# Optimization experiments

Measured on AMD Instinct MI355X. Metric: run time of the kernel, lower is better.

Reference implementation:

```python
import jax, jax.numpy as jnp
import numpy as np

# DeepSpeed FixedSparsityConfig defaults (attention='unidirectional')
BLOCK = 16
NUM_LOCAL_BLOCKS = 4   # local window = 4 blocks = 64 tokens
D_MODEL = 1024
N_HEADS = 16
HEAD_DIM = D_MODEL // N_HEADS


def _block_layout(seq_len: int) -> np.ndarray:
    """Token-level boolean mask [S,S] from the fixed unidirectional block layout.
    Allowed iff: (same 4-block local window AND block_k <= block_q) OR
                 (block_k % 4 == 3 AND block_k <= block_q)  (causal global column).
    Same layout for every head (different_layout_per_head=False)."""
    nb = seq_len // BLOCK
    r = np.arange(nb)
    causal = r[None, :] <= r[:, None]
    same_win = (r[:, None] // NUM_LOCAL_BLOCKS) == (r[None, :] // NUM_LOCAL_BLOCKS)
    glob = (r[None, :] % NUM_LOCAL_BLOCKS) == (NUM_LOCAL_BLOCKS - 1)
    layout = (same_win & causal) | (glob & causal)
    return np.kron(layout, np.ones((BLOCK, BLOCK), dtype=bool))


def setup_inputs() -> dict:
    key = jax.random.key(0)
    ks = jax.random.split(key, 7)
    B, S = 2, 2048
    init = 1.0 / np.sqrt(D_MODEL)
    x = jax.random.normal(ks[0], (B, S, D_MODEL), jnp.float32)
    key_padding_mask = jnp.zeros((B, S), jnp.float32)  # additive mask ('add' mode)
    Wq = jax.random.normal(ks[1], (D_MODEL, D_MODEL), jnp.float32) * init
    Wk = jax.random.normal(ks[2], (D_MODEL, D_MODEL), jnp.float32) * init
    Wv = jax.random.normal(ks[3], (D_MODEL, D_MODEL), jnp.float32) * init
    bq = jax.random.normal(ks[4], (D_MODEL,), jnp.float32) * 0.01
    bk = jax.random.normal(ks[5], (D_MODEL,), jnp.float32) * 0.01
    bv = jax.random.normal(ks[6], (D_MODEL,), jnp.float32) * 0.01
    return dict(x=x, key_padding_mask=key_padding_mask,
                Wq=Wq, bq=bq, Wk=Wk, bk=bk, Wv=Wv, bv=bv)


def reference(x, key_padding_mask, Wq, bq, Wk, bk, Wv, bv):
    B, S, D = x.shape
    q = (x @ Wq + bq).reshape(B, S, N_HEADS, HEAD_DIM)
    k = (x @ Wk + bk).reshape(B, S, N_HEADS, HEAD_DIM)
    v = (x @ Wv + bv).reshape(B, S, N_HEADS, HEAD_DIM)
    scale = HEAD_DIM ** -0.5  # DeepSpeed scales by head_size**-0.5 inside softmax
    scores = jnp.einsum('bqhd,bkhd->bhqk', q, k) * scale
    scores = scores + key_padding_mask[:, None, None, :]
    mask = jnp.asarray(_block_layout(S))  # [S,S] bool; absent blocks excluded from softmax
    scores = jnp.where(mask[None, None], scores, -jnp.inf)
    attn = jax.nn.softmax(scores, axis=-1)
    out = jnp.einsum('bhqk,bkhd->bqhd', attn, v)
    return out.reshape(B, S, D)
```

## Files before the change

kernel.cpp:

```cpp
#include <hip/hip_runtime.h>
#include <hip/hip_bf16.h>

typedef __bf16 bf16;
typedef __bf16 bf16x4 __attribute__((ext_vector_type(4)));
typedef __bf16 bf16x8 __attribute__((ext_vector_type(8)));
typedef float  f32x4  __attribute__((ext_vector_type(4)));

#define D_MODEL 1024
#define S_LEN   2048
#define BATCH   2
#define NH      16
#define HD      64
#define NX ((size_t)BATCH * S_LEN * D_MODEL)

__device__ inline void gl_lds16(const bf16* g, bf16* l) {
    __builtin_amdgcn_global_load_lds(
        (const __attribute__((address_space(1))) void*)g,
        (__attribute__((address_space(3))) void*)l, 16, 0, 0);
}

__global__ __launch_bounds__(256) void prep(
    const float* __restrict__ x, bf16* __restrict__ xb,
    const float* __restrict__ Wq, const float* __restrict__ Wk,
    const float* __restrict__ Wv, bf16* __restrict__ Wt)
{
    __shared__ bf16 tile[64 * 72];

    if (blockIdx.x < 2048) {
        const size_t base = ((size_t)blockIdx.x * 256 + threadIdx.x) * 8;
        const float4 a = *(const float4*)(x + base);
        const float4 b = *(const float4*)(x + base + 4);
        bf16x8 o;
        o[0] = (bf16)a.x; o[1] = (bf16)a.y; o[2] = (bf16)a.z; o[3] = (bf16)a.w;
        o[4] = (bf16)b.x; o[5] = (bf16)b.y; o[6] = (bf16)b.z; o[7] = (bf16)b.w;
        *(bf16x8*)(xb + base) = o;
        return;
    }

    const int id2 = blockIdx.x - 2048;
    const int z = id2 >> 8;
    const float* W = (z == 0) ? Wq : (z == 1) ? Wk : Wv;
    const int k0 = ((id2 >> 4) & 15) * 64, n0 = (id2 & 15) * 64;

    const int r16 = threadIdx.x >> 4, c4 = (threadIdx.x & 15) << 2;

#pragma unroll
    for (int rr = 0; rr < 4; ++rr) {
        const int row = rr * 16 + r16;
        const float4 v = *(const float4*)(W + (size_t)(k0 + row) * D_MODEL + n0 + c4);
        bf16x4 o; o[0] = (bf16)v.x; o[1] = (bf16)v.y; o[2] = (bf16)v.z; o[3] = (bf16)v.w;
        *(bf16x4*)(tile + row * 72 + c4) = o;
    }
    __syncthreads();
#pragma unroll
    for (int rr = 0; rr < 4; ++rr) {
        const int row = rr * 16 + r16;
        bf16x4 o;
#pragma unroll
        for (int j = 0; j < 4; ++j) o[j] = tile[(c4 + j) * 72 + row];
        *(bf16x4*)(Wt + (size_t)(z * D_MODEL + n0 + row) * D_MODEL + k0 + c4) = o;
    }
}

#define GNT 32

__device__ __forceinline__ void stage_128(
    const bf16* __restrict__ src, bf16* __restrict__ dst,
    int row0, int k0, int tid, int wave)
{
    const int ci0 = tid;
    const int r0 = ci0 >> 2, c0 = (ci0 & 3) ^ ((ci0 >> 3) & 3);
    gl_lds16(src + (size_t)(row0 + r0) * D_MODEL + k0 + c0 * 8, dst + wave * 512);
    const int ci1 = 256 + tid;
    const int r1 = ci1 >> 2, c1 = (ci1 & 3) ^ ((ci1 >> 3) & 3);
    gl_lds16(src + (size_t)(row0 + r1) * D_MODEL + k0 + c1 * 8, dst + 2048 + wave * 512);
}

template<int VM>
__device__ __forceinline__ void gemm_tile_body(
    const bf16* __restrict__ Xb, const bf16* __restrict__ Wt,
    bf16* __restrict__ As, bf16* __restrict__ Bs,
    int m0, int n0, int t, int tid, int wave, int wm, int wn,
    int col, int pchunk, f32x4 (&acc)[4][4])
{
    __builtin_amdgcn_sched_barrier(0);
    if constexpr (VM == 4) asm volatile("s_waitcnt vmcnt(4)");
    else                   asm volatile("s_waitcnt vmcnt(0)");
    __builtin_amdgcn_sched_barrier(0);
    __builtin_amdgcn_s_barrier();
    __builtin_amdgcn_sched_barrier(0);

    const int cur = t % 3;
    const bf16* bufA = As + cur * 4096;
    const bf16* bufB = Bs + cur * 4096;

    if (t + 2 < GNT) {
        const int nslot = (t + 2) % 3;
        const int k2 = (t + 2) * 32;
        stage_128(Xb, As + nslot * 4096, m0, k2, tid, wave);
        stage_128(Wt, Bs + nslot * 4096, n0, k2, tid, wave);
    }

    bf16x8 a[4], b[4];
#pragma unroll
    for (int mr = 0; mr < 4; ++mr)
        a[mr] = *(const bf16x8*)(bufA + (wm * 64 + mr * 16 + col) * 32 + pchunk * 8);
#pragma unroll
    for (int nr = 0; nr < 4; ++nr)
        b[nr] = *(const bf16x8*)(bufB + (wn * 64 + nr * 16 + col) * 32 + pchunk * 8);

#pragma unroll
    for (int mr = 0; mr < 4; ++mr)
#pragma unroll
        for (int nr = 0; nr < 4; ++nr)
            acc[mr][nr] = __builtin_amdgcn_mfma_f32_16x16x32_bf16(a[mr], b[nr], acc[mr][nr], 0, 0, 0);
}

__global__ __launch_bounds__(256, 3) void gemm_qkv_dp(
    const bf16* __restrict__ Xb, const bf16* __restrict__ Wt,
    const float* __restrict__ bq, const float* __restrict__ bk,
    const float* __restrict__ bv, bf16* __restrict__ QKV)
{
    extern __shared__ bf16 smem[];
    bf16* As = smem;
    bf16* Bs = smem + 12288;

    const int bid = blockIdx.x, k = bid & 7, j = bid >> 3;
    const int my = ((k & 3) << 3) + (j & 7);
    const int nx = ((k >> 2) * 12) + (j >> 3);
    const int m0 = my * 128, n0 = nx * 128;

    const int tid = threadIdx.x, wave = tid >> 6, lane = tid & 63;
    const int wm = wave >> 1, wn = wave & 1;
    const int col = lane & 15, quad = lane >> 4;
    const int pchunk = quad ^ ((col >> 1) & 3);

    f32x4 acc[4][4] = {};

    stage_128(Xb, As,        m0,  0, tid, wave);
    stage_128(Wt, Bs,        n0,  0, tid, wave);
    stage_128(Xb, As + 4096, m0, 32, tid, wave);
    stage_128(Wt, Bs + 4096, n0, 32, tid, wave);

    for (int t = 0; t < GNT - 1; ++t)
        gemm_tile_body<4>(Xb, Wt, As, Bs, m0, n0, t, tid, wave, wm, wn, col, pchunk, acc);
    gemm_tile_body<0>(Xb, Wt, As, Bs, m0, n0, GNT - 1, tid, wave, wm, wn, col, pchunk, acc);

    const int z = n0 >> 10, nc0 = n0 & 1023;
    const float* bias = (z == 0) ? bq : (z == 1) ? bk : bv;
    const float scale = (z == 0) ? 0.125f : 1.0f;
    bf16* C = QKV + (size_t)z * NX;
#pragma unroll
    for (int nr = 0; nr < 4; ++nr) {
        const int c = nc0 + wn * 64 + nr * 16 + col;
        const float bsv = bias[c];
#pragma unroll
        for (int mr = 0; mr < 4; ++mr)
#pragma unroll
            for (int i = 0; i < 4; ++i) {
                const int rg = m0 + wm * 64 + mr * 16 + quad * 4 + i;
                C[(size_t)rg * D_MODEL + c] = (bf16)((acc[mr][nr][i] + bsv) * scale);
            }
    }
}

__global__ __launch_bounds__(256, 4) void sparse_attn64(
    const bf16* __restrict__ Q, const bf16* __restrict__ Kv,
    const bf16* __restrict__ Vv, const float* __restrict__ kpm,
    float* __restrict__ out)
{
    const int lid = blockIdx.x + 32 * (blockIdx.y + 16 * blockIdx.z);
    const int xk = lid & 7, j = lid >> 3;
    const int pair = xk * 4 + (j & 3);
    const int h = pair & 15, b = pair >> 4;
    const int w = 31 - (j >> 2);

    const int t = threadIdx.x, wavei = t >> 6, lane = t & 63;
    const int col = lane & 15, quad = lane >> 4;
    const int qb = 4 * w + wavei;

    __shared__ bf16 KbS[64 * 72];
    __shared__ bf16 VtS[2][64 * 72];
    __shared__ bf16 Ps[4][16 * 72];

    const size_t qrow = ((size_t)(b * S_LEN + qb * 16 + col)) * D_MODEL + h * HD;
    const bf16x8 aq0 = *(const bf16x8*)(Q + qrow + quad * 8);
    const bf16x8 aq1 = *(const bf16x8*)(Q + qrow + 32 + quad * 8);

    f32x4 o[4] = {};
    float lacc[4] = {0.f, 0.f, 0.f, 0.f};

    const int nGlob = (w + 3) >> 2;
    const int niter = nGlob + 1;

    const int srow = t >> 2, sd16 = (t & 3) << 4;
    const int sg = srow >> 4, sr = srow & 15;
    const int p2 = t & 31, dg8 = (t >> 5) << 3;
    const int key0 = 2 * p2, vg = key0 >> 4, vr = key0 & 15;

    auto kb_of = [&](int it, int g) -> int {
        if (it >= nGlob) return 4 * w + g;
        const int jj = 4 * it + g;
        return (jj < w) ? (4 * jj + 3) : 3;
    };

    bf16x8 rk0, rk1, rv0, rv1;
    {
        const size_t krow = ((size_t)(b * S_LEN + kb_of(0, sg) * 16 + sr)) * D_MODEL + h * HD + sd16;
        rk0 = *(const bf16x8*)(Kv + krow);
        rk1 = *(const bf16x8*)(Kv + krow + 8);
        const size_t vrow = ((size_t)(b * S_LEN + kb_of(0, vg) * 16 + vr)) * D_MODEL + h * HD + dg8;
        rv0 = *(const bf16x8*)(Vv + vrow);
        rv1 = *(const bf16x8*)(Vv + vrow + D_MODEL);
        *(bf16x8*)(KbS + srow * 72 + sd16)     = rk0;
        *(bf16x8*)(KbS + srow * 72 + sd16 + 8) = rk1;
#pragma unroll
        for (int jj = 0; jj < 8; ++jj) {
            bf16 pr[2] = { rv0[jj], rv1[jj] };
            *(unsigned int*)(VtS[0] + (dg8 + jj) * 72 + key0) = *(unsigned int*)pr;
        }
    }

    for (int it = 0; it < niter; ++it) {
        __syncthreads();
        const int cur = it & 1, nxt = cur ^ 1;
        const bool more = (it + 1 < niter);
        if (more) {
            const size_t krow = ((size_t)(b * S_LEN + kb_of(it + 1, sg) * 16 + sr)) * D_MODEL + h * HD + sd16;
            rk0 = *(const bf16x8*)(Kv + krow);
            rk1 = *(const bf16x8*)(Kv + krow + 8);
            const size_t vrow = ((size_t)(b * S_LEN + kb_of(it + 1, vg) * 16 + vr)) * D_MODEL + h * HD + dg8;
            rv0 = *(const bf16x8*)(Vv + vrow);
            rv1 = *(const bf16x8*)(Vv + vrow + D_MODEL);
        }

        f32x4 s[4];
        float mval[4];
        bool  val[4];
#pragma unroll
        for (int g = 0; g < 4; ++g) {
            val[g] = (it == nGlob) ? (g <= wavei) : (4 * it + g < w);
            if (val[g]) {
                const int kb = kb_of(it, g);
                mval[g] = kpm[b * S_LEN + kb * 16 + col];
                f32x4 z = {};
                const bf16x8 bk0 = *(const bf16x8*)(KbS + (g * 16 + col) * 72 + quad * 8);
                const bf16x8 bk1 = *(const bf16x8*)(KbS + (g * 16 + col) * 72 + 32 + quad * 8);
                __builtin_amdgcn_s_setprio(1);
                z = __builtin_amdgcn_mfma_f32_16x16x32_bf16(aq0, bk0, z, 0, 0, 0);
                s[g] = __builtin_amdgcn_mfma_f32_16x16x32_bf16(aq1, bk1, z, 0, 0, 0);
                __builtin_amdgcn_s_setprio(0);
            }
        }

        __syncthreads();
        if (more) {
            *(bf16x8*)(KbS + srow * 72 + sd16)     = rk0;
            *(bf16x8*)(KbS + srow * 72 + sd16 + 8) = rk1;
        }

#pragma unroll
        for (int g = 0; g < 4; ++g) {
            if (val[g]) {
#pragma unroll
                for (int i = 0; i < 4; ++i) {
                    const float pv = __expf(s[g][i] + mval[g]);
                    lacc[i] += pv;
                    Ps[wavei][(quad * 4 + i) * 72 + g * 16 + col] = (bf16)pv;
                }
            } else {
#pragma unroll
                for (int i = 0; i < 4; ++i)
                    Ps[wavei][(quad * 4 + i) * 72 + g * 16 + col] = (bf16)0.0f;
            }
        }

        const bf16* Vt = VtS[cur];
        const bf16x8 aP0 = *(const bf16x8*)(Ps[wavei] + col * 72 + quad * 8);
        const bf16x8 aP1 = *(const bf16x8*)(Ps[wavei] + col * 72 + 32 + quad * 8);
        __builtin_amdgcn_s_setprio(1);
#pragma unroll
        for (int nt = 0; nt < 4; ++nt) {
            const bf16x8 b0 = *(const bf16x8*)(Vt + (nt * 16 + col) * 72 + quad * 8);
            const bf16x8 b1 = *(const bf16x8*)(Vt + (nt * 16 + col) * 72 + 32 + quad * 8);
            o[nt] = __builtin_amdgcn_mfma_f32_16x16x32_bf16(aP0, b0, o[nt], 0, 0, 0);
            o[nt] = __builtin_amdgcn_mfma_f32_16x16x32_bf16(aP1, b1, o[nt], 0, 0, 0);
        }
        __builtin_amdgcn_s_setprio(0);

        if (more) {
#pragma unroll
            for (int jj = 0; jj < 8; ++jj) {
                bf16 pr[2] = { rv0[jj], rv1[jj] };
                *(unsigned int*)(VtS[nxt] + (dg8 + jj) * 72 + key0) = *(unsigned int*)pr;
            }
        }
    }

#pragma unroll
    for (int i = 0; i < 4; ++i) {
        float rs = lacc[i];
        rs += __shfl_xor(rs, 1);
        rs += __shfl_xor(rs, 2);
        rs += __shfl_xor(rs, 4);
        rs += __shfl_xor(rs, 8);
        const float inv = 1.0f / rs;
        const int rg = b * S_LEN + qb * 16 + quad * 4 + i;
#pragma unroll
        for (int nt = 0; nt < 4; ++nt)
            out[(size_t)rg * D_MODEL + h * HD + nt * 16 + col] = o[nt][i] * inv;
    }
}

extern "C" void kernel_launch(void* const* d_in, const int* in_sizes, int n_in,
                              void* d_out, int out_size, void* d_ws, size_t ws_size,
                              hipStream_t stream)
{
    const float* x = nullptr; const float* kpm = nullptr;
    const float* Wp[3] = {nullptr, nullptr, nullptr};
    const float* bp[3] = {nullptr, nullptr, nullptr};
    int wn = 0, bn = 0;
    for (int i = 0; i < n_in; ++i) {
        const float* p = (const float*)d_in[i];
        const long s = in_sizes[i];
        if (s == (long)NX)            x = p;
        else if (s == BATCH * S_LEN)  kpm = p;
        else if (s == D_MODEL * D_MODEL && wn < 3) Wp[wn++] = p;
        else if (s == D_MODEL && bn < 3)           bp[bn++] = p;
    }

    bf16* Qb = (bf16*)d_ws;
    bf16* Kb = Qb + NX;
    bf16* Vb = Kb + NX;
    bf16* Xb = (bf16*)d_out;
    bf16* Wt = Xb + NX;
    float* outp = (float*)d_out;

    static bool attr_done = false;
    if (!attr_done) {
        (void)hipFuncSetAttribute(reinterpret_cast<const void*>(gemm_qkv_dp),
                                  hipFuncAttributeMaxDynamicSharedMemorySize, 49152);
        attr_done = true;
    }

    prep<<<2816, 256, 0, stream>>>(x, Xb, Wp[0], Wp[1], Wp[2], Wt);

    gemm_qkv_dp<<<dim3(768), 256, 49152, stream>>>(
        Xb, Wt, bp[0], bp[1], bp[2], Qb);

    sparse_attn64<<<dim3(S_LEN / 64, NH, BATCH), 256, 0, stream>>>(
        Qb, Kb, Vb, kpm, outp);
}
```

Before: 141.8 us.

## Enlarge QKV GEMM tile to 256x192 so the grid fits one wave of CUs

```diff
diff --git a/kernel.cpp b/kernel.cpp
--- a/kernel.cpp
+++ b/kernel.cpp
@@ -64,16 +64,30 @@
 
 #define GNT 32
 
-__device__ __forceinline__ void stage_128(
+__device__ __forceinline__ void stage_A256(
     const bf16* __restrict__ src, bf16* __restrict__ dst,
     int row0, int k0, int tid, int wave)
 {
-    const int ci0 = tid;
-    const int r0 = ci0 >> 2, c0 = (ci0 & 3) ^ ((ci0 >> 3) & 3);
-    gl_lds16(src + (size_t)(row0 + r0) * D_MODEL + k0 + c0 * 8, dst + wave * 512);
-    const int ci1 = 256 + tid;
-    const int r1 = ci1 >> 2, c1 = (ci1 & 3) ^ ((ci1 >> 3) & 3);
-    gl_lds16(src + (size_t)(row0 + r1) * D_MODEL + k0 + c1 * 8, dst + 2048 + wave * 512);
+#pragma unroll
+    for (int p = 0; p < 4; ++p) {
+        const int ci = p * 256 + tid;
+        const int r = ci >> 2, c = (ci & 3) ^ ((ci >> 3) & 3);
+        gl_lds16(src + (size_t)(row0 + r) * D_MODEL + k0 + c * 8,
+                 dst + p * 2048 + wave * 512);
+    }
+}
+
+__device__ __forceinline__ void stage_B192(
+    const bf16* __restrict__ src, bf16* __restrict__ dst,
+    int row0, int k0, int tid, int wave)
+{
+#pragma unroll
+    for (int p = 0; p < 3; ++p) {
+        const int ci = p * 256 + tid;
+        const int r = ci >> 2, c = (ci & 3) ^ ((ci >> 3) & 3);
+        gl_lds16(src + (size_t)(row0 + r) * D_MODEL + k0 + c * 8,
+                 dst + p * 2048 + wave * 512);
+    }
 }
 
 template<int VM>
@@ -81,84 +95,82 @@
     const bf16* __restrict__ Xb, const bf16* __restrict__ Wt,
     bf16* __restrict__ As, bf16* __restrict__ Bs,
     int m0, int n0, int t, int tid, int wave, int wm, int wn,
-    int col, int pchunk, f32x4 (&acc)[4][4])
+    int col, int pchunk, f32x4 (&acc)[8][6])
 {
     __builtin_amdgcn_sched_barrier(0);
-    if constexpr (VM == 4) asm volatile("s_waitcnt vmcnt(4)");
+    if constexpr (VM == 7) asm volatile("s_waitcnt vmcnt(7)");
     else                   asm volatile("s_waitcnt vmcnt(0)");
     __builtin_amdgcn_sched_barrier(0);
     __builtin_amdgcn_s_barrier();
     __builtin_amdgcn_sched_barrier(0);
 
-    const int cur = t % 3;
-    const bf16* bufA = As + cur * 4096;
-    const bf16* bufB = Bs + cur * 4096;
+    const bf16* bufA = As + (t % 3) * 8192;
+    const bf16* bufB = Bs + (t % 3) * 6144;
 
     if (t + 2 < GNT) {
         const int nslot = (t + 2) % 3;
         const int k2 = (t + 2) * 32;
-        stage_128(Xb, As + nslot * 4096, m0, k2, tid, wave);
-        stage_128(Wt, Bs + nslot * 4096, n0, k2, tid, wave);
-    }
-
-    bf16x8 a[4], b[4];
-#pragma unroll
-    for (int mr = 0; mr < 4; ++mr)
-        a[mr] = *(const bf16x8*)(bufA + (wm * 64 + mr * 16 + col) * 32 + pchunk * 8);
-#pragma unroll
-    for (int nr = 0; nr < 4; ++nr)
-        b[nr] = *(const bf16x8*)(bufB + (wn * 64 + nr * 16 + col) * 32 + pchunk * 8);
-
-#pragma unroll
-    for (int mr = 0; mr < 4; ++mr)
-#pragma unroll
-        for (int nr = 0; nr < 4; ++nr)
+        stage_A256(Xb, As + nslot * 8192, m0, k2, tid, wave);
+        stage_B192(Wt, Bs + nslot * 6144, n0, k2, tid, wave);
+    }
+
+    bf16x8 a[8], b[6];
+#pragma unroll
+    for (int mr = 0; mr < 8; ++mr)
+        a[mr] = *(const bf16x8*)(bufA + (wm * 128 + mr * 16 + col) * 32 + pchunk * 8);
+#pragma unroll
+    for (int nr = 0; nr < 6; ++nr)
+        b[nr] = *(const bf16x8*)(bufB + (wn * 96 + nr * 16 + col) * 32 + pchunk * 8);
+
+#pragma unroll
+    for (int mr = 0; mr < 8; ++mr)
+#pragma unroll
+        for (int nr = 0; nr < 6; ++nr)
             acc[mr][nr] = __builtin_amdgcn_mfma_f32_16x16x32_bf16(a[mr], b[nr], acc[mr][nr], 0, 0, 0);
 }
 
-__global__ __launch_bounds__(256, 3) void gemm_qkv_dp(
+__global__ __launch_bounds__(256, 1) void gemm_qkv_dp(
     const bf16* __restrict__ Xb, const bf16* __restrict__ Wt,
     const float* __restrict__ bq, const float* __restrict__ bk,
     const float* __restrict__ bv, bf16* __restrict__ QKV)
 {
     extern __shared__ bf16 smem[];
     bf16* As = smem;
-    bf16* Bs = smem + 12288;
+    bf16* Bs = smem + 24576;
 
     const int bid = blockIdx.x, k = bid & 7, j = bid >> 3;
-    const int my = ((k & 3) << 3) + (j & 7);
-    const int nx = ((k >> 2) * 12) + (j >> 3);
-    const int m0 = my * 128, n0 = nx * 128;
+    const int my = ((k & 3) << 2) + (j >> 3);
+    const int nx = ((k >> 2) << 3) + (j & 7);
+    const int m0 = my * 256, n0 = nx * 192;
 
     const int tid = threadIdx.x, wave = tid >> 6, lane = tid & 63;
     const int wm = wave >> 1, wn = wave & 1;
     const int col = lane & 15, quad = lane >> 4;
     const int pchunk = quad ^ ((col >> 1) & 3);
 
-    f32x4 acc[4][4] = {};
-
-    stage_128(Xb, As,        m0,  0, tid, wave);
-    stage_128(Wt, Bs,        n0,  0, tid, wave);
-    stage_128(Xb, As + 4096, m0, 32, tid, wave);
-    stage_128(Wt, Bs + 4096, n0, 32, tid, wave);
+    f32x4 acc[8][6] = {};
+
+    stage_A256(Xb, As,        m0,  0, tid, wave);
+    stage_B192(Wt, Bs,        n0,  0, tid, wave);
+    stage_A256(Xb, As + 8192, m0, 32, tid, wave);
+    stage_B192(Wt, Bs + 6144, n0, 32, tid, wave);
 
     for (int t = 0; t < GNT - 1; ++t)
-        gemm_tile_body<4>(Xb, Wt, As, Bs, m0, n0, t, tid, wave, wm, wn, col, pchunk, acc);
+        gemm_tile_body<7>(Xb, Wt, As, Bs, m0, n0, t, tid, wave, wm, wn, col, pchunk, acc);
     gemm_tile_body<0>(Xb, Wt, As, Bs, m0, n0, GNT - 1, tid, wave, wm, wn, col, pchunk, acc);
 
-    const int z = n0 >> 10, nc0 = n0 & 1023;
-    const float* bias = (z == 0) ? bq : (z == 1) ? bk : bv;
-    const float scale = (z == 0) ? 0.125f : 1.0f;
-    bf16* C = QKV + (size_t)z * NX;
-#pragma unroll
-    for (int nr = 0; nr < 4; ++nr) {
-        const int c = nc0 + wn * 64 + nr * 16 + col;
-        const float bsv = bias[c];
-#pragma unroll
-        for (int mr = 0; mr < 4; ++mr)
+#pragma unroll
+    for (int nr = 0; nr < 6; ++nr) {
+        const int cg = n0 + wn * 96 + nr * 16 + col;
+        const int z = cg >> 10, c = cg & 1023;
+        const float bsv = (z == 0 ? bq : (z == 1 ? bk : bv))[c];
+        const float scale = (z == 0) ? 0.125f : 1.0f;
+        bf16* C = QKV + (size_t)z * NX;
+#pragma unroll
+        for (int mr = 0; mr < 8; ++mr)
 #pragma unroll
             for (int i = 0; i < 4; ++i) {
-                const int rg = m0 + wm * 64 + mr * 16 + quad * 4 + i;
+                const int rg = m0 + wm * 128 + mr * 16 + quad * 4 + i;
                 C[(size_t)rg * D_MODEL + c] = (bf16)((acc[mr][nr][i] + bsv) * scale);
             }
     }
@@ -339,13 +351,13 @@
     static bool attr_done = false;
     if (!attr_done) {
         (void)hipFuncSetAttribute(reinterpret_cast<const void*>(gemm_qkv_dp),
-                                  hipFuncAttributeMaxDynamicSharedMemorySize, 49152);
+                                  hipFuncAttributeMaxDynamicSharedMemorySize, 86016);
         attr_done = true;
     }
 
     prep<<<2816, 256, 0, stream>>>(x, Xb, Wp[0], Wp[1], Wp[2], Wt);
 
-    gemm_qkv_dp<<<dim3(768), 256, 49152, stream>>>(
+    gemm_qkv_dp<<<dim3(256), 256, 86016, stream>>>(
         Xb, Wt, bp[0], bp[1], bp[2], Qb);
 
     sparse_attn64<<<dim3(S_LEN / 64, NH, BATCH), 256, 0, stream>>>(
```

Result: no change. 139.9 us (-1.3%).
